# Kernel optimization log

Hardware: AMD Instinct MI355X
Metric: run time of the kernel (lower is better)

The kernel has to match this reference:

```python
import jax, jax.numpy as jnp
import numpy as np

B, S, D = 2, 2048, 2048
H, KVH, HD = 32, 8, 64
GROUPS = H // KVH  # 4
NEG = -1e9


def setup_inputs() -> dict:
    key = jax.random.key(0)
    ks = jax.random.split(key, 5)
    x = jax.random.normal(ks[0], (B, S, D), dtype=jnp.float32)
    # causal additive mask [1,1,S,S]
    causal = jnp.triu(jnp.full((S, S), NEG, dtype=jnp.float32), k=1)[None, None]
    Wq = jax.random.normal(ks[1], (D, D), dtype=jnp.float32) * (D ** -0.5)
    Wk = jax.random.normal(ks[2], (KVH * HD, D), dtype=jnp.float32) * (D ** -0.5)
    Wv = jax.random.normal(ks[3], (KVH * HD, D), dtype=jnp.float32) * (D ** -0.5)
    Wo = jax.random.normal(ks[4], (D, D), dtype=jnp.float32) * (D ** -0.5)
    return {"x": x, "attention_mask": causal, "Wq": Wq, "Wk": Wk, "Wv": Wv, "Wo": Wo}


def reference(x, attention_mask, Wq, Wk, Wv, Wo):
    b, s, _ = x.shape
    # projections (nn.Linear: y = x @ W.T)
    q = (x @ Wq.T).reshape(b, s, H, HD).transpose(0, 2, 1, 3)      # [b,H,s,hd]
    k = (x @ Wk.T).reshape(b, s, KVH, HD).transpose(0, 2, 1, 3)    # [b,KVH,s,hd]
    v = (x @ Wv.T).reshape(b, s, KVH, HD).transpose(0, 2, 1, 3)
    new_kv_cache = (k, v)
    # repeat_interleave over head dim for GQA
    k = jnp.repeat(k, GROUPS, axis=1)  # [b,H,s,hd]
    v = jnp.repeat(v, GROUPS, axis=1)
    scale = 1.0 / jnp.sqrt(jnp.float32(HD))
    scores = jnp.einsum('bhqd,bhkd->bhqk', q, k) * scale
    scores = scores + attention_mask
    attn = jax.nn.softmax(scores.astype(jnp.float32), axis=-1).astype(q.dtype)
    out = jnp.einsum('bhqk,bhkd->bhqd', attn, v)  # [b,H,s,hd]
    out = out.transpose(0, 2, 1, 3).reshape(b, s, H * HD)
    output = out @ Wo.T
    return (output, new_kv_cache[0], new_kv_cache[1])
```

## Files before the change

kernel.cpp:

```cpp
#include <hip/hip_runtime.h>
#include <hip/hip_bf16.h>
#include <stdint.h>

#define B_ 2
#define S_ 2048
#define D_ 2048
#define H_ 32
#define KVH_ 8
#define HD_ 64

typedef __bf16 bf16x8 __attribute__((ext_vector_type(8)));
typedef float f32x4 __attribute__((ext_vector_type(4)));

#define MFMA16(a, b, c) __builtin_amdgcn_mfma_f32_16x16x32_bf16((a), (b), (c), 0, 0, 0)

typedef __attribute__((address_space(1))) void gvoid_t;
typedef __attribute__((address_space(3))) void lvoid_t;

__device__ __forceinline__ void async_ld16(__hip_bfloat16* lds, const __hip_bfloat16* g) {
  __builtin_amdgcn_global_load_lds((gvoid_t*)(void*)(g), (lvoid_t*)(lds), 16, 0, 0);
}

__device__ __forceinline__ unsigned short f2bu(float f) {
  __hip_bfloat16 h = __float2bfloat16(f);
  return *reinterpret_cast<unsigned short*>(&h);
}

__global__ void cast_all_kernel(const float* __restrict__ x,
                                const float* __restrict__ wq,
                                const float* __restrict__ wk,
                                const float* __restrict__ wv,
                                const float* __restrict__ wo,
                                unsigned short* __restrict__ xb,
                                unsigned short* __restrict__ wqkvb,
                                unsigned short* __restrict__ wob) {
  constexpr int NX = B_ * S_ * D_ / 4;
  constexpr int NQ = D_ * D_ / 4;
  constexpr int NK = KVH_ * HD_ * D_ / 4;
  constexpr int E0 = NX;
  constexpr int E1 = E0 + NQ;
  constexpr int E2 = E1 + NK;
  constexpr int E3 = E2 + NK;
  constexpr int E4 = E3 + NQ;
  const int stride = gridDim.x * blockDim.x;
  for (int i = blockIdx.x * blockDim.x + threadIdx.x; i < E4; i += stride) {
    const float* src; unsigned short* dst; int j;
    if (i < E0)      { src = x;  dst = xb;                              j = i; }
    else if (i < E1) { src = wq; dst = wqkvb;                           j = i - E0; }
    else if (i < E2) { src = wk; dst = wqkvb + (size_t)2048 * D_;       j = i - E1; }
    else if (i < E3) { src = wv; dst = wqkvb + (size_t)2560 * D_;       j = i - E2; }
    else             { src = wo; dst = wob;                             j = i - E3; }
    float4 v = reinterpret_cast<const float4*>(src)[j];
    ushort4 o;
    o.x = f2bu(v.x); o.y = f2bu(v.y); o.z = f2bu(v.z); o.w = f2bu(v.w);
    reinterpret_cast<ushort4*>(dst)[j] = o;
  }
}

template <int MODE>
__global__ __launch_bounds__(256, 2)
void gemm_bt(const __hip_bfloat16* __restrict__ A,
             const __hip_bfloat16* __restrict__ W,
             float* __restrict__ Cf, __hip_bfloat16* __restrict__ Cb,
             float* __restrict__ Cf2, __hip_bfloat16* __restrict__ Cb2,
             __hip_bfloat16* __restrict__ Cb3,
             int M, int N, int K) {
  __shared__ __align__(16) __hip_bfloat16 sA[128 * 64];
  __shared__ __align__(16) __hip_bfloat16 sB[128 * 64];
  const int tid = threadIdx.x;
  const int lane = tid & 63;
  const int wv = tid >> 6;
  const int l15 = lane & 15, l4 = lane >> 4;

  const int nwg = gridDim.x * gridDim.y;
  const int lid = blockIdx.y * gridDim.x + blockIdx.x;
  const int swz = (lid & 7) * (nwg >> 3) + (lid >> 3);
  const int bm = (swz % gridDim.x) * 128;
  const int bn = (swz / gridDim.x) * 128;

  const int wm = (wv >> 1) * 64, wn = (wv & 1) * 64;

  const __hip_bfloat16* gA[4];
  const __hip_bfloat16* gB[4];
#pragma unroll
  for (int i = 0; i < 4; ++i) {
    const int ci = tid + i * 256;
    const int row = ci >> 3;
    const int lc = (ci & 7) ^ (row & 7);
    gA[i] = A + (size_t)(bm + row) * K + lc * 8;
    gB[i] = W + (size_t)(bn + row) * K + lc * 8;
  }

  f32x4 acc[4][4];
#pragma unroll
  for (int i = 0; i < 4; ++i) {
#pragma unroll
    for (int j = 0; j < 4; ++j) acc[i][j] = f32x4{0.f, 0.f, 0.f, 0.f};
  }

  for (int k0 = 0; k0 < K; k0 += 64) {
#pragma unroll
    for (int i = 0; i < 4; ++i) {
      async_ld16(&sA[(tid + i * 256) * 8], gA[i] + k0);
      async_ld16(&sB[(tid + i * 256) * 8], gB[i] + k0);
    }
    __syncthreads();
#pragma unroll
    for (int kk = 0; kk < 2; ++kk) {
      bf16x8 af[4], bfr[4];
#pragma unroll
      for (int i = 0; i < 4; ++i) {
        const int row = wm + i * 16 + l15;
        af[i] = *reinterpret_cast<const bf16x8*>(
            &sA[row * 64 + (((kk * 4 + l4) ^ (row & 7)) * 8)]);
      }
#pragma unroll
      for (int j = 0; j < 4; ++j) {
        const int row = wn + j * 16 + l15;
        bfr[j] = *reinterpret_cast<const bf16x8*>(
            &sB[row * 64 + (((kk * 4 + l4) ^ (row & 7)) * 8)]);
      }
#pragma unroll
      for (int i = 0; i < 4; ++i) {
#pragma unroll
        for (int j = 0; j < 4; ++j) acc[i][j] = MFMA16(af[i], bfr[j], acc[i][j]);
      }
    }
    __syncthreads();
  }

#pragma unroll
  for (int i = 0; i < 4; ++i) {
#pragma unroll
    for (int j = 0; j < 4; ++j) {
      const int col = bn + wn + j * 16 + l15;
#pragma unroll
      for (int r = 0; r < 4; ++r) {
        const int row = bm + wm + i * 16 + l4 * 4 + r;
        const float v = acc[i][j][r];
        if (MODE == 1) {
          Cf[(size_t)row * N + col] = v;
        } else {
          if (bn < 2048) {
            Cb[(size_t)row * 2048 + col] = __float2bfloat16(v);
          } else {
            const int bb = row >> 11, s = row & 2047;
            const int kv = col - 2048;
            if (kv < 512) {
              const int g = kv >> 6, hd = kv & 63;
              const size_t idx = ((size_t)(bb * KVH_ + g) * S_ + s) * HD_ + hd;
              Cf[idx] = v;
              Cb2[idx] = __float2bfloat16(v);
            } else {
              const int vv = kv - 512;
              const int g = vv >> 6, hd = vv & 63;
              const size_t idx = ((size_t)(bb * KVH_ + g) * S_ + s) * HD_ + hd;
              Cf2[idx] = v;
              Cb3[((size_t)(bb * KVH_ + g) * HD_ + hd) * S_ + s] = __float2bfloat16(v);
            }
          }
        }
      }
    }
  }
}

__global__ __launch_bounds__(512, 4)
void attn_fused(const __hip_bfloat16* __restrict__ Qb,
                const __hip_bfloat16* __restrict__ Kb,
                const __hip_bfloat16* __restrict__ Vtb,
                __hip_bfloat16* __restrict__ AOb) {
  __shared__ __align__(16) __hip_bfloat16 sK[2][64 * 64];
  __shared__ __align__(16) __hip_bfloat16 sV[2][64 * 64];
  __shared__ __align__(16) __hip_bfloat16 sP[8 * 16 * 64];

  const int tid = threadIdx.x;
  const int lane = tid & 63;
  const int wv = tid >> 6;
  const int l15 = lane & 15, l4 = lane >> 4;
  const int h = blockIdx.x & 31;
  const int b = blockIdx.x >> 5;
  const int qt = 15 - blockIdx.y;
  const int g = h >> 2;

  bf16x8 qf[2];
  {
    const __hip_bfloat16* Qp =
        Qb + ((size_t)(b * S_ + qt * 128 + wv * 16 + l15)) * D_ + h * HD_;
#pragma unroll
    for (int c = 0; c < 2; ++c)
      qf[c] = *reinterpret_cast<const bf16x8*>(Qp + c * 32 + l4 * 8);
  }

  f32x4 oacc[4];
  f32x4 lacc = f32x4{0.f, 0.f, 0.f, 0.f};
#pragma unroll
  for (int j = 0; j < 4; ++j) oacc[j] = f32x4{0.f, 0.f, 0.f, 0.f};

  bf16x8 vone;
#pragma unroll
  for (int j = 0; j < 8; ++j) vone[j] = (__bf16)1.0f;

  const __hip_bfloat16* Kp = Kb + (size_t)(b * KVH_ + g) * S_ * HD_;
  const __hip_bfloat16* Vp = Vtb + (size_t)(b * KVH_ + g) * HD_ * S_;
  __hip_bfloat16* sPw = sP + wv * (16 * 64);
  const float CE = 0.125f * 1.4426950408889634f;
  const float MSUB = 8.0f;

  const int r0 = tid >> 3, c0 = (tid & 7) ^ (r0 & 7);
  const __hip_bfloat16* gk = Kp + (size_t)r0 * HD_ + c0 * 8;
  const __hip_bfloat16* gv = Vp + (size_t)r0 * S_ + c0 * 8;

  auto stage = [&](int buf) {
    async_ld16(&sK[buf][tid * 8], gk);
    async_ld16(&sV[buf][tid * 8], gv);
    gk += 64 * HD_;
    gv += 64;
  };

  auto pack = [&](f32x4 (&sc)[4], int koff) {
    if (koff >= 0) {
#pragma unroll
      for (int jn = 0; jn < 4; ++jn) {
        const int kp = koff + jn * 16 + l15;
#pragma unroll
        for (int r = 0; r < 4; ++r) {
          const int qp = wv * 16 + l4 * 4 + r;
          if (kp > qp) sc[jn][r] = -3.0e38f;
        }
      }
    }
#pragma unroll
    for (int jj = 0; jj < 4; ++jj) {
#pragma unroll
      for (int r = 0; r < 4; ++r) {
        const float p = exp2f(fmaf(sc[jj][r], CE, -MSUB));
        sPw[(l4 * 4 + r) * 64 + ((jj ^ l4) * 16 + l15)] = __float2bfloat16(p);
      }
    }
  };

  const int nsteps = 2 * qt + 2;
  stage(0);
  for (int ki = 0; ki < nsteps; ++ki) {
    const int cur = ki & 1;
    __syncthreads();
    if (ki + 1 < nsteps) stage(cur ^ 1);
    const int ko = ((ki >> 1) == qt) ? (ki & 1) * 64 : -1;

    f32x4 sc[4];
    __builtin_amdgcn_s_setprio(1);
#pragma unroll
    for (int jn = 0; jn < 4; ++jn) {
      const int row = jn * 16 + l15;
      const bf16x8 k0 = *reinterpret_cast<const bf16x8*>(
          &sK[cur][(row * 8 + (l4 ^ (row & 7))) * 8]);
      const bf16x8 k1 = *reinterpret_cast<const bf16x8*>(
          &sK[cur][(row * 8 + ((4 + l4) ^ (row & 7))) * 8]);
      f32x4 t = f32x4{0.f, 0.f, 0.f, 0.f};
      t = MFMA16(qf[0], k0, t);
      t = MFMA16(qf[1], k1, t);
      sc[jn] = t;
    }
    __builtin_amdgcn_s_setprio(0);

    pack(sc, ko);

    const int gr = (l15 >> 2) & 3;
    __builtin_amdgcn_s_setprio(1);
#pragma unroll
    for (int kc = 0; kc < 2; ++kc) {
      bf16x8 vf[4];
#pragma unroll
      for (int jn = 0; jn < 4; ++jn) {
        const int row = jn * 16 + l15;
        vf[jn] = *reinterpret_cast<const bf16x8*>(
            &sV[cur][(row * 8 + ((kc * 4 + l4) ^ (row & 7))) * 8]);
      }
      const int pcol = (((kc * 2 + (l4 >> 1)) ^ gr) * 16 + (l4 & 1) * 8);
      const bf16x8 pf = *reinterpret_cast<const bf16x8*>(&sPw[l15 * 64 + pcol]);
#pragma unroll
      for (int jn = 0; jn < 4; ++jn) oacc[jn] = MFMA16(pf, vf[jn], oacc[jn]);
      lacc = MFMA16(pf, vone, lacc);
    }
    __builtin_amdgcn_s_setprio(0);
  }

  float inv[4];
#pragma unroll
  for (int r = 0; r < 4; ++r) inv[r] = 1.0f / lacc[r];
#pragma unroll
  for (int jn = 0; jn < 4; ++jn) {
#pragma unroll
    for (int r = 0; r < 4; ++r) {
      const int qp = qt * 128 + wv * 16 + l4 * 4 + r;
      AOb[(size_t)(b * S_ + qp) * D_ + h * HD_ + jn * 16 + l15] =
          __float2bfloat16(oacc[jn][r] * inv[r]);
    }
  }
}

extern "C" void kernel_launch(void* const* d_in, const int* in_sizes, int n_in,
                              void* d_out, int out_size, void* d_ws, size_t ws_size,
                              hipStream_t stream) {
  (void)in_sizes; (void)n_in; (void)out_size; (void)ws_size;
  const float* x = (const float*)d_in[0];
  const float* Wq = (const float*)d_in[2];
  const float* Wk = (const float*)d_in[3];
  const float* Wv = (const float*)d_in[4];
  const float* Wo = (const float*)d_in[5];

  float* outO = (float*)d_out;
  float* outK = outO + (size_t)B_ * S_ * D_;
  float* outV = outK + (size_t)B_ * KVH_ * S_ * HD_;

  char* p = (char*)d_ws;
  __hip_bfloat16* xb    = (__hip_bfloat16*)p; p += (size_t)B_ * S_ * D_ * 2;
  __hip_bfloat16* Wqkvb = (__hip_bfloat16*)p; p += (size_t)3072 * D_ * 2;
  __hip_bfloat16* Wob   = (__hip_bfloat16*)p; p += (size_t)D_ * D_ * 2;
  __hip_bfloat16* Qbf   = (__hip_bfloat16*)p; p += (size_t)B_ * S_ * D_ * 2;
  __hip_bfloat16* Kbf   = (__hip_bfloat16*)p; p += (size_t)B_ * KVH_ * S_ * HD_ * 2;
  __hip_bfloat16* Vtb   = (__hip_bfloat16*)p; p += (size_t)B_ * KVH_ * S_ * HD_ * 2;
  __hip_bfloat16* AOb   = (__hip_bfloat16*)p; p += (size_t)B_ * S_ * D_ * 2;

  cast_all_kernel<<<dim3(4096), dim3(256), 0, stream>>>(
      x, Wq, Wk, Wv, Wo,
      (unsigned short*)xb, (unsigned short*)Wqkvb, (unsigned short*)Wob);

  gemm_bt<4><<<dim3(32, 24), dim3(256), 0, stream>>>(
      xb, Wqkvb, outK, Qbf, outV, Kbf, Vtb, 4096, 3072, 2048);
  attn_fused<<<dim3(64, 16, 1), dim3(512), 0, stream>>>(Qbf, Kbf, Vtb, AOb);
  gemm_bt<1><<<dim3(32, 16), dim3(256), 0, stream>>>(
      AOb, Wob, outO, nullptr, nullptr, nullptr, nullptr, 4096, 2048, 2048);
}
```

Baseline: 312.1 us.

## Split long causal query tiles across two KV ranges and merge partials

The attention grid grows from 16 to 24 query-tile slots per (batch, head). Each of the eight longest causal tiles (8..15) is split into two blocks that cover the lower and upper halves of its KV range, with a packed lookup table deciding tile order and split index. Split blocks write unnormalised fp32 partial outputs and row sums into reused scratch regions (the bf16 x buffer and the final output buffer). A new reduce kernel then sums the two partials, normalises them and writes bf16. The goal is to cut the load imbalance and tail of the causal attention pass, at the cost of an extra launch and extra fp32 partial traffic.

```diff
diff --git a/kernel.cpp b/kernel.cpp
--- a/kernel.cpp
+++ b/kernel.cpp
@@ -169,7 +169,9 @@
 void attn_fused(const __hip_bfloat16* __restrict__ Qb,
                 const __hip_bfloat16* __restrict__ Kb,
                 const __hip_bfloat16* __restrict__ Vtb,
-                __hip_bfloat16* __restrict__ AOb) {
+                __hip_bfloat16* __restrict__ AOb,
+                float* __restrict__ O0, float* __restrict__ L0,
+                float* __restrict__ O1, float* __restrict__ L1) {
   __shared__ __align__(16) __hip_bfloat16 sK[2][64 * 64];
   __shared__ __align__(16) __hip_bfloat16 sV[2][64 * 64];
   __shared__ __align__(16) __hip_bfloat16 sP[8 * 16 * 64];
@@ -180,7 +182,13 @@
   const int l15 = lane & 15, l4 = lane >> 4;
   const int h = blockIdx.x & 31;
   const int b = blockIdx.x >> 5;
-  const int qt = 15 - blockIdx.y;
+  const int y = blockIdx.y;
+  const int qt = (y < 16) ? (int)((0x9AA5BBCC6DDEE7FFull >> (y * 4)) & 15)
+                          : (int)((0x01238849u >> ((y - 16) * 4)) & 15);
+  const int sp = (int)((0xAA4912449124ull >> (y * 2)) & 3);
+  const int k0s = (sp == 1) ? (qt + 1) : 0;
+  const int k1s = (sp == 0) ? (qt + 1) : (2 * qt + 2);
+  const int ns = k1s - k0s;
   const int g = h >> 2;
 
   bf16x8 qf[2];
@@ -208,8 +216,8 @@
   const float MSUB = 8.0f;
 
   const int r0 = tid >> 3, c0 = (tid & 7) ^ (r0 & 7);
-  const __hip_bfloat16* gk = Kp + (size_t)r0 * HD_ + c0 * 8;
-  const __hip_bfloat16* gv = Vp + (size_t)r0 * S_ + c0 * 8;
+  const __hip_bfloat16* gk = Kp + (size_t)(k0s * 64 + r0) * HD_ + c0 * 8;
+  const __hip_bfloat16* gv = Vp + (size_t)r0 * S_ + k0s * 64 + c0 * 8;
 
   auto stage = [&](int buf) {
     async_ld16(&sK[buf][tid * 8], gk);
@@ -240,12 +248,12 @@
     }
   };
 
-  const int nsteps = 2 * qt + 2;
   stage(0);
-  for (int ki = 0; ki < nsteps; ++ki) {
-    const int cur = ki & 1;
+  for (int s = 0; s < ns; ++s) {
+    const int ki = k0s + s;
+    const int cur = s & 1;
     __syncthreads();
-    if (ki + 1 < nsteps) stage(cur ^ 1);
+    if (s + 1 < ns) stage(cur ^ 1);
     const int ko = ((ki >> 1) == qt) ? (ki & 1) * 64 : -1;
 
     f32x4 sc[4];
@@ -286,18 +294,61 @@
     __builtin_amdgcn_s_setprio(0);
   }
 
-  float inv[4];
-#pragma unroll
-  for (int r = 0; r < 4; ++r) inv[r] = 1.0f / lacc[r];
-#pragma unroll
-  for (int jn = 0; jn < 4; ++jn) {
-#pragma unroll
-    for (int r = 0; r < 4; ++r) {
-      const int qp = qt * 128 + wv * 16 + l4 * 4 + r;
-      AOb[(size_t)(b * S_ + qp) * D_ + h * HD_ + jn * 16 + l15] =
-          __float2bfloat16(oacc[jn][r] * inv[r]);
-    }
-  }
+  if (sp == 2) {
+    float inv[4];
+#pragma unroll
+    for (int r = 0; r < 4; ++r) inv[r] = 1.0f / lacc[r];
+#pragma unroll
+    for (int jn = 0; jn < 4; ++jn) {
+#pragma unroll
+      for (int r = 0; r < 4; ++r) {
+        const int qp = qt * 128 + wv * 16 + l4 * 4 + r;
+        AOb[(size_t)(b * S_ + qp) * D_ + h * HD_ + jn * 16 + l15] =
+            __float2bfloat16(oacc[jn][r] * inv[r]);
+      }
+    }
+  } else {
+    float* Ob = sp ? O1 : O0;
+    float* Lb = sp ? L1 : L0;
+    const int bh = blockIdx.x;
+    const size_t rbase = (size_t)(bh * 8 + (qt - 8)) * 128 + wv * 16 + l4 * 4;
+#pragma unroll
+    for (int jn = 0; jn < 4; ++jn) {
+#pragma unroll
+      for (int r = 0; r < 4; ++r)
+        Ob[(rbase + r) * 64 + jn * 16 + l15] = oacc[jn][r];
+    }
+    if (l15 == 0) {
+#pragma unroll
+      for (int r = 0; r < 4; ++r) Lb[rbase + r] = lacc[r];
+    }
+  }
+}
+
+__global__ void attn_reduce(const float* __restrict__ O0,
+                            const float* __restrict__ L0,
+                            const float* __restrict__ O1,
+                            const float* __restrict__ L1,
+                            __hip_bfloat16* __restrict__ AOb) {
+  const int i = blockIdx.x * 256 + threadIdx.x;
+  const int d4 = i & 15;
+  const int row = (i >> 4) & 127;
+  const int qi = (i >> 11) & 7;
+  const int bh = i >> 14;
+  const int b = bh >> 5, h = bh & 31;
+  const size_t po = (((size_t)(bh * 8 + qi) * 128 + row) * 64) + d4 * 4;
+  const size_t pl = (size_t)(bh * 8 + qi) * 128 + row;
+  const float4 a = *reinterpret_cast<const float4*>(O0 + po);
+  const float4 c = *reinterpret_cast<const float4*>(O1 + po);
+  const float inv = 1.0f / (L0[pl] + L1[pl]);
+  const int qp = (qi + 8) * 128 + row;
+  ushort4 o;
+  o.x = f2bu((a.x + c.x) * inv);
+  o.y = f2bu((a.y + c.y) * inv);
+  o.z = f2bu((a.z + c.z) * inv);
+  o.w = f2bu((a.w + c.w) * inv);
+  *reinterpret_cast<ushort4*>(
+      (unsigned short*)AOb + ((size_t)(b * S_ + qp)) * D_ + h * HD_ + d4 * 4) = o;
 }
 
 extern "C" void kernel_launch(void* const* d_in, const int* in_sizes, int n_in,
@@ -323,13 +374,19 @@
   __hip_bfloat16* Vtb   = (__hip_bfloat16*)p; p += (size_t)B_ * KVH_ * S_ * HD_ * 2;
   __hip_bfloat16* AOb   = (__hip_bfloat16*)p; p += (size_t)B_ * S_ * D_ * 2;
 
+  constexpr size_t PART_ELEMS = (size_t)64 * 8 * 128 * 64;
+  float* O0 = (float*)d_ws;          float* L0 = O0 + PART_ELEMS;
+  float* O1 = outO;                  float* L1 = O1 + PART_ELEMS;
+
   cast_all_kernel<<<dim3(4096), dim3(256), 0, stream>>>(
       x, Wq, Wk, Wv, Wo,
       (unsigned short*)xb, (unsigned short*)Wqkvb, (unsigned short*)Wob);
 
   gemm_bt<4><<<dim3(32, 24), dim3(256), 0, stream>>>(
       xb, Wqkvb, outK, Qbf, outV, Kbf, Vtb, 4096, 3072, 2048);
-  attn_fused<<<dim3(64, 16, 1), dim3(512), 0, stream>>>(Qbf, Kbf, Vtb, AOb);
+  attn_fused<<<dim3(64, 24, 1), dim3(512), 0, stream>>>(
+      Qbf, Kbf, Vtb, AOb, O0, L0, O1, L1);
+  attn_reduce<<<dim3(4096), dim3(256), 0, stream>>>(O0, L0, O1, L1, AOb);
   gemm_bt<1><<<dim3(32, 16), dim3(256), 0, stream>>>(
       AOb, Wob, outO, nullptr, nullptr, nullptr, nullptr, 4096, 2048, 2048);
 }
```

Result: no change. 313.4 us (+0.4%).
